# Kernel tuning notes

Measured on AMD Instinct MI355X. Metric: run time of the kernel, lower is better.

The kernel has to match this reference:

```python
import jax, jax.numpy as jnp
import numpy as np

TOP_K = 2
EPS = 1e-20


def setup_inputs() -> dict:
    key = jax.random.key(0)
    ks = jax.random.split(key, 8)
    B, S, H, E, D = 4, 2048, 1024, 8, 2048
    s = 0.02
    return {
        "x":  jax.random.normal(ks[0], (B, S, H), dtype=jnp.float32),
        "Wr": jax.random.normal(ks[1], (H, E), dtype=jnp.float32) * s,
        "Wg": jax.random.normal(ks[2], (E, H, D), dtype=jnp.float32) * s,
        "Wu": jax.random.normal(ks[3], (E, H, D), dtype=jnp.float32) * s,
        "Wd": jax.random.normal(ks[4], (E, D, H), dtype=jnp.float32) * s,
        "Sg": jax.random.normal(ks[5], (H, D), dtype=jnp.float32) * s,
        "Su": jax.random.normal(ks[6], (H, D), dtype=jnp.float32) * s,
        "Sd": jax.random.normal(ks[7], (D, H), dtype=jnp.float32) * s,
    }


def reference(x, Wr, Wg, Wu, Wd, Sg, Su, Sd):
    B, S, H = x.shape
    T = B * S
    xt = x.reshape(T, H)

    # Router: softmax scores, top-k, renormalize top-k weights
    scores = jax.nn.softmax(xt @ Wr, axis=-1)            # [T, E]
    topk_w, topk_idx = jax.lax.top_k(scores, TOP_K)      # [T, K]
    topk_w = topk_w / (topk_w.sum(axis=-1, keepdims=True) + EPS)

    # Per-expert SwiGLU FFN computed densely over all tokens (vectorized over E)
    g = jax.nn.silu(jnp.einsum('th,ehd->etd', xt, Wg))   # [E, T, D]
    u = jnp.einsum('th,ehd->etd', xt, Wu)                # [E, T, D]
    out_all = jnp.einsum('etd,edh->eth', g * u, Wd)      # [E, T, H]

    # Combine: gather each token's top-k expert outputs, weighted sum
    tok = jnp.arange(T)[:, None]                          # [T, 1]
    gathered = out_all[topk_idx, tok, :]                  # [T, K, H]
    out = jnp.sum(gathered * topk_w[..., None], axis=1).reshape(B, S, H)

    # Shared expert (applied to original input, added to MoE output)
    shared = (jax.nn.silu(x @ Sg) * (x @ Su)) @ Sd        # [B, S, H]
    return out + shared
```

## Files before the change

### kernel.cpp

```cpp
#include <hip/hip_runtime.h>
#include <stdint.h>

#define T_TOK 8192
#define HD 1024
#define ED 8
#define DD 2048
#define BM 128
#define BK 32
#define TILE_SHARED 64
#define TILE_MAX 200
#define ROWCAP 25600
#define RT_TPW 8

typedef short short8 __attribute__((ext_vector_type(8)));
typedef float f32x4 __attribute__((ext_vector_type(4)));

__device__ __forceinline__ unsigned short f2bf(float f) {
  union { float f; unsigned int u; } v; v.f = f;
  unsigned int r = (v.u + 0x7fffu + ((v.u >> 16) & 1u)) >> 16;
  return (unsigned short)r;
}

__device__ __forceinline__ void gll16(const void* g, void* l) {
  __builtin_amdgcn_global_load_lds(
      (const __attribute__((address_space(1))) unsigned int*)g,
      (__attribute__((address_space(3))) unsigned int*)l, 16, 0, 0);
}

__global__ __launch_bounds__(256) void k_zero(float* __restrict__ outp) {
  size_t i = (size_t)blockIdx.x * 256 + threadIdx.x;
  ((float4*)outp)[i] = make_float4(0.f, 0.f, 0.f, 0.f);
}

__global__ __launch_bounds__(256) void k_init(int* counts, int* tok, float* wrow) {
  int i = blockIdx.x * 256 + threadIdx.x;
  if (i < 32) counts[i] = 0;
  if (i < ROWCAP) {
    tok[i] = (i < T_TOK) ? i : 0;
    wrow[i] = (i < T_TOK) ? 1.0f : 0.0f;
  }
}

__global__ __launch_bounds__(256) void k_transpose(const float* __restrict__ in,
    unsigned short* __restrict__ outp, int R, int C) {
  __shared__ float tile[32][33];
  size_t boff = (size_t)blockIdx.z * (size_t)R * (size_t)C;
  in += boff; outp += boff;
  int c0 = blockIdx.x * 32, r0 = blockIdx.y * 32;
  int tx = threadIdx.x & 31, ty = threadIdx.x >> 5;
#pragma unroll
  for (int i = 0; i < 4; ++i)
    tile[ty + i * 8][tx] = in[(size_t)(r0 + ty + i * 8) * C + c0 + tx];
  __syncthreads();
#pragma unroll
  for (int i = 0; i < 4; ++i)
    outp[(size_t)(c0 + ty + i * 8) * R + r0 + tx] = f2bf(tile[tx][ty + i * 8]);
}

__global__ __launch_bounds__(256) void k_router(const float* __restrict__ x,
    const float* __restrict__ Wr, unsigned short* __restrict__ xb,
    int* __restrict__ counts, int* __restrict__ topE, float* __restrict__ topW) {
  __shared__ float wrT[ED * HD];
  __shared__ int hist[ED];
  int tid = threadIdx.x;
  if (tid < ED) hist[tid] = 0;
  for (int i = tid; i < ED * HD; i += 256) {
    int e = i >> 10, h = i & (HD - 1);
    wrT[i] = Wr[h * ED + e];
  }
  __syncthreads();
  int lane = tid & 63, wave = tid >> 6;
  int tbase = (blockIdx.x * 4 + wave) * RT_TPW;
  for (int tt = 0; tt < RT_TPW; ++tt) {
    int t = tbase + tt;
    const float* xrow = x + (size_t)t * HD;
    unsigned short* xbrow = xb + (size_t)t * HD;
    float acc[ED] = {0, 0, 0, 0, 0, 0, 0, 0};
#pragma unroll
    for (int i = 0; i < HD / 64; ++i) {
      int h = i * 64 + lane;
      float v = xrow[h];
      xbrow[h] = f2bf(v);
#pragma unroll
      for (int e = 0; e < ED; ++e) acc[e] += v * wrT[e * HD + h];
    }
#pragma unroll
    for (int off = 32; off; off >>= 1)
#pragma unroll
      for (int e = 0; e < ED; ++e) acc[e] += __shfl_xor(acc[e], off);
    if (lane == 0) {
      float m = acc[0];
#pragma unroll
      for (int e = 1; e < ED; ++e) m = fmaxf(m, acc[e]);
      float p[ED], s = 0.f;
#pragma unroll
      for (int e = 0; e < ED; ++e) { p[e] = __expf(acc[e] - m); s += p[e]; }
      int i0 = 0;
#pragma unroll
      for (int e = 1; e < ED; ++e) if (acc[e] > acc[i0]) i0 = e;
      int i1 = -1;
#pragma unroll
      for (int e = 0; e < ED; ++e) {
        if (e == i0) continue;
        if (i1 < 0 || acc[e] > acc[i1]) i1 = e;
      }
      float p0 = p[i0] / s, p1 = p[i1] / s;
      float rs = p0 + p1 + 1e-20f;
      topE[t * 2] = i0; topE[t * 2 + 1] = i1;
      topW[t * 2] = p0 / rs; topW[t * 2 + 1] = p1 / rs;
      atomicAdd(&hist[i0], 1);
      atomicAdd(&hist[i1], 1);
    }
  }
  __syncthreads();
  if (tid < ED) atomicAdd(&counts[tid], hist[tid]);
}

__global__ __launch_bounds__(256) void k_plan(const int* __restrict__ counts, int* cursor,
    int* __restrict__ tileE, int* __restrict__ tileEnd) {
  __shared__ int tstart[ED + 1], segend[ED];
  if (threadIdx.x == 0) {
    int base = T_TOK, rt = TILE_SHARED;
    for (int e = 0; e < ED; ++e) {
      int c = counts[e];
      cursor[e] = base;
      tstart[e] = rt;
      segend[e] = base + c;
      int tiles = (c + BM - 1) >> 7;
      rt += tiles;
      base += tiles << 7;
    }
    tstart[ED] = rt;
  }
  __syncthreads();
  for (int rt = threadIdx.x; rt < TILE_MAX; rt += 256) {
    int e = -1, end = 0;
    if (rt < TILE_SHARED) { e = ED; end = T_TOK; }
    else {
      for (int q = 0; q < ED; ++q)
        if (rt >= tstart[q] && rt < tstart[q + 1]) { e = q; end = segend[q]; }
    }
    tileE[rt] = e; tileEnd[rt] = end;
  }
}

__global__ __launch_bounds__(256) void k_scatter(const int* __restrict__ topE,
    const float* __restrict__ topW, int* cursor, int* tok, float* wrow) {
  __shared__ int lcount[ED], lbase[ED];
  int tid = threadIdx.x;
  if (tid < ED) lcount[tid] = 0;
  __syncthreads();
  int t = blockIdx.x * 256 + tid;
  int e0 = topE[t * 2], e1 = topE[t * 2 + 1];
  float w0 = topW[t * 2], w1 = topW[t * 2 + 1];
  int s0 = atomicAdd(&lcount[e0], 1);
  int s1 = atomicAdd(&lcount[e1], 1);
  __syncthreads();
  if (tid < ED) lbase[tid] = atomicAdd(&cursor[tid], lcount[tid]);
  __syncthreads();
  int p0 = lbase[e0] + s0;
  int p1 = lbase[e1] + s1;
  tok[p0] = t; wrow[p0] = w0;
  tok[p1] = t; wrow[p1] = w1;
}


__global__ __launch_bounds__(256, 2) void k_gemm1(
    const unsigned short* __restrict__ xb,
    const unsigned short* __restrict__ wgt, const unsigned short* __restrict__ wut,
    const unsigned short* __restrict__ sgt, const unsigned short* __restrict__ sut,
    const int* __restrict__ tok, const int* __restrict__ tileE,
    const int* __restrict__ tileEnd, unsigned short* __restrict__ hbuf, int tileBase) {
  int lt = blockIdx.y;
  int rt = tileBase + lt;
  int e = tileE[rt];
  if (e < 0) return;
  int n0 = blockIdx.x * BM;
  int grow0 = rt * BM;
  int hrow0 = lt * BM;
  int segEnd = tileEnd[rt];
  const unsigned short* bg = (e == ED) ? sgt : wgt + (size_t)e * DD * HD;
  const unsigned short* bu = (e == ED) ? sut : wut + (size_t)e * DD * HD;

  __shared__ __align__(16) unsigned short As[2][BM * BK];
  __shared__ __align__(16) unsigned short Bg[2][BM * BK];
  __shared__ __align__(16) unsigned short Bu[2][BM * BK];

  int tid = threadIdx.x, lane = tid & 63, wave = tid >> 6;
  int wm = (wave & 1) * 64, wn = (wave >> 1) * 64;
  int kc = (lane & 3) ^ ((lane >> 3) & 3);

  int ldsU[2];
  const unsigned short *pA[2], *pBg[2], *pBu[2];
#pragma unroll
  for (int r = 0; r < 2; ++r) {
    int chunk = r * 4 + wave;
    int row = chunk * 16 + (lane >> 2);
    ldsU[r] = chunk * 512;
    pA[r]  = xb + (size_t)tok[grow0 + row] * HD + kc * 8;
    pBg[r] = bg + (size_t)(n0 + row) * HD + kc * 8;
    pBu[r] = bu + (size_t)(n0 + row) * HD + kc * 8;
  }

  f32x4 zero = {0.f, 0.f, 0.f, 0.f};
  f32x4 accg[4][4], accu[4][4];
#pragma unroll
  for (int i = 0; i < 4; ++i)
#pragma unroll
    for (int j = 0; j < 4; ++j) { accg[i][j] = zero; accu[i][j] = zero; }

  int m15 = lane & 15;
  int sl8 = (((lane >> 4) ^ ((lane >> 1) & 3)) * 8);

#pragma unroll
  for (int r = 0; r < 2; ++r) {
    gll16(pA[r],  &As[0][ldsU[r]]);
    gll16(pBg[r], &Bg[0][ldsU[r]]);
    gll16(pBu[r], &Bu[0][ldsU[r]]);
  }
  __syncthreads();

  for (int k0 = 0; k0 < HD; k0 += BK) {
    int b = (k0 >> 5) & 1;
    int k1 = k0 + BK;
    if (k1 < HD) {
#pragma unroll
      for (int r = 0; r < 2; ++r) {
        gll16(pA[r] + k1,  &As[b ^ 1][ldsU[r]]);
        gll16(pBg[r] + k1, &Bg[b ^ 1][ldsU[r]]);
        gll16(pBu[r] + k1, &Bu[b ^ 1][ldsU[r]]);
      }
    }
    __builtin_amdgcn_sched_barrier(0);
    short8 af[4], bgf[4], buf_[4];
#pragma unroll
    for (int i = 0; i < 4; ++i) {
      af[i]   = *(const short8*)(&As[b][(wm + i * 16 + m15) * BK + sl8]);
      bgf[i]  = *(const short8*)(&Bg[b][(wn + i * 16 + m15) * BK + sl8]);
      buf_[i] = *(const short8*)(&Bu[b][(wn + i * 16 + m15) * BK + sl8]);
    }
#pragma unroll
    for (int i = 0; i < 4; ++i)
#pragma unroll
      for (int j = 0; j < 4; ++j) {
        accg[i][j] = __builtin_amdgcn_mfma_f32_16x16x32_bf16(af[i], bgf[j],  accg[i][j], 0, 0, 0);
        accu[i][j] = __builtin_amdgcn_mfma_f32_16x16x32_bf16(af[i], buf_[j], accu[i][j], 0, 0, 0);
      }
    __syncthreads();
  }

  int colB = n0 + wn + m15;
  int rowB = wm + ((lane >> 4) << 2);
#pragma unroll
  for (int i = 0; i < 4; ++i)
#pragma unroll
    for (int j = 0; j < 4; ++j)
#pragma unroll
      for (int r = 0; r < 4; ++r) {
        int lr = rowB + i * 16 + r;
        float g = accg[i][j][r], u = accu[i][j][r];
        float h = (grow0 + lr < segEnd) ? (g / (1.0f + __expf(-g))) * u : 0.0f;
        hbuf[(size_t)(hrow0 + lr) * DD + colB + j * 16] = f2bf(h);
      }
}

__global__ __launch_bounds__(256, 2) void k_gemm2(
    const unsigned short* __restrict__ hbuf,
    const unsigned short* __restrict__ wdt, const unsigned short* __restrict__ sdt,
    const int* __restrict__ tok, const int* __restrict__ tileE,
    const int* __restrict__ tileEnd, const float* __restrict__ wrow,
    float* __restrict__ outp, int tileBase) {
  int lt = blockIdx.y;
  int rt = tileBase + lt;
  int e = tileE[rt];
  if (e < 0) return;
  int n0 = blockIdx.x * BM;
  int grow0 = rt * BM;
  int hrow0 = lt * BM;
  int segEnd = tileEnd[rt];
  const unsigned short* bd = (e == ED) ? sdt : wdt + (size_t)e * HD * DD;

  __shared__ __align__(16) unsigned short As[2][BM * BK];
  __shared__ __align__(16) unsigned short Bs[2][BM * BK];

  int tid = threadIdx.x, lane = tid & 63, wave = tid >> 6;
  int wm = (wave & 1) * 64, wn = (wave >> 1) * 64;
  int kc = (lane & 3) ^ ((lane >> 3) & 3);

  int ldsU[2];
  const unsigned short *pA[2], *pB[2];
#pragma unroll
  for (int r = 0; r < 2; ++r) {
    int chunk = r * 4 + wave;
    int row = chunk * 16 + (lane >> 2);
    ldsU[r] = chunk * 512;
    pA[r] = hbuf + (size_t)(hrow0 + row) * DD + kc * 8;
    pB[r] = bd + (size_t)(n0 + row) * DD + kc * 8;
  }

  f32x4 zero = {0.f, 0.f, 0.f, 0.f};
  f32x4 acc[4][4];
#pragma unroll
  for (int i = 0; i < 4; ++i)
#pragma unroll
    for (int j = 0; j < 4; ++j) acc[i][j] = zero;

  int m15 = lane & 15;
  int sl8 = (((lane >> 4) ^ ((lane >> 1) & 3)) * 8);

#pragma unroll
  for (int r = 0; r < 2; ++r) {
    gll16(pA[r], &As[0][ldsU[r]]);
    gll16(pB[r], &Bs[0][ldsU[r]]);
  }
  __syncthreads();

  for (int k0 = 0; k0 < DD; k0 += BK) {
    int b = (k0 >> 5) & 1;
    int k1 = k0 + BK;
    if (k1 < DD) {
#pragma unroll
      for (int r = 0; r < 2; ++r) {
        gll16(pA[r] + k1, &As[b ^ 1][ldsU[r]]);
        gll16(pB[r] + k1, &Bs[b ^ 1][ldsU[r]]);
      }
    }
    __builtin_amdgcn_sched_barrier(0);
    short8 af[4], bf[4];
#pragma unroll
    for (int i = 0; i < 4; ++i) {
      af[i] = *(const short8*)(&As[b][(wm + i * 16 + m15) * BK + sl8]);
      bf[i] = *(const short8*)(&Bs[b][(wn + i * 16 + m15) * BK + sl8]);
    }
#pragma unroll
    for (int i = 0; i < 4; ++i)
#pragma unroll
      for (int j = 0; j < 4; ++j)
        acc[i][j] = __builtin_amdgcn_mfma_f32_16x16x32_bf16(af[i], bf[j], acc[i][j], 0, 0, 0);
    __syncthreads();
  }

  int colB = n0 + wn + m15;
  int rowB = wm + ((lane >> 4) << 2);
#pragma unroll
  for (int i = 0; i < 4; ++i)
#pragma unroll
    for (int r = 0; r < 4; ++r) {
      int grr = grow0 + rowB + i * 16 + r;
      if (grr < segEnd) {
        float w = wrow[grr];
        size_t ob = (size_t)tok[grr] * HD;
#pragma unroll
        for (int j = 0; j < 4; ++j)
          atomicAdd(&outp[ob + colB + j * 16], acc[i][j][r] * w);
      }
    }
}

extern "C" void kernel_launch(void* const* d_in, const int* in_sizes, int n_in,
                              void* d_out, int out_size, void* d_ws, size_t ws_size,
                              hipStream_t stream) {
  const float* x  = (const float*)d_in[0];
  const float* Wr = (const float*)d_in[1];
  const float* Wg = (const float*)d_in[2];
  const float* Wu = (const float*)d_in[3];
  const float* Wd = (const float*)d_in[4];
  const float* Sg = (const float*)d_in[5];
  const float* Su = (const float*)d_in[6];
  const float* Sd = (const float*)d_in[7];
  float* outp = (float*)d_out;

  size_t fixed = 0;
  auto pad = [](size_t b) { return (b + 255) & ~(size_t)255; };
  fixed += pad((size_t)T_TOK * HD * 2);
  fixed += pad((size_t)ED * DD * HD * 2) * 3;
  fixed += pad((size_t)DD * HD * 2) * 3;
  fixed += pad((size_t)ROWCAP * 4) * 2;
  fixed += pad((size_t)T_TOK * 2 * 4) * 2;
  fixed += pad(128) * 2 + pad(1024) * 2;
  int CH = TILE_MAX;
  if (fixed + pad((size_t)CH * BM * DD * 2) > ws_size) CH = TILE_MAX / 2;
  if (fixed + pad((size_t)CH * BM * DD * 2) > ws_size) return;

  char* ws = (char*)d_ws;
  size_t off = 0;
  auto alloc = [&](size_t bytes) -> char* {
    char* p = ws + off;
    off += (bytes + 255) & ~(size_t)255;
    return p;
  };
  unsigned short* xb  = (unsigned short*)alloc((size_t)T_TOK * HD * 2);
  unsigned short* wgt = (unsigned short*)alloc((size_t)ED * DD * HD * 2);
  unsigned short* wut = (unsigned short*)alloc((size_t)ED * DD * HD * 2);
  unsigned short* wdt = (unsigned short*)alloc((size_t)ED * HD * DD * 2);
  unsigned short* sgt = (unsigned short*)alloc((size_t)DD * HD * 2);
  unsigned short* sut = (unsigned short*)alloc((size_t)DD * HD * 2);
  unsigned short* sdt = (unsigned short*)alloc((size_t)HD * DD * 2);
  int* tok       = (int*)alloc((size_t)ROWCAP * 4);
  float* wrow    = (float*)alloc((size_t)ROWCAP * 4);
  int* topE      = (int*)alloc((size_t)T_TOK * 2 * 4);
  float* topW    = (float*)alloc((size_t)T_TOK * 2 * 4);
  int* counts    = (int*)alloc(128);
  int* cursor    = (int*)alloc(128);
  int* tileE     = (int*)alloc(1024);
  int* tileEnd   = (int*)alloc(1024);
  unsigned short* hbuf = (unsigned short*)alloc((size_t)CH * BM * DD * 2);

  k_zero<<<(out_size / 4 + 255) / 256, 256, 0, stream>>>(outp);
  k_init<<<(ROWCAP + 255) / 256, 256, 0, stream>>>(counts, tok, wrow);
  k_transpose<<<dim3(DD / 32, HD / 32, ED), 256, 0, stream>>>(Wg, wgt, HD, DD);
  k_transpose<<<dim3(DD / 32, HD / 32, ED), 256, 0, stream>>>(Wu, wut, HD, DD);
  k_transpose<<<dim3(HD / 32, DD / 32, ED), 256, 0, stream>>>(Wd, wdt, DD, HD);
  k_transpose<<<dim3(DD / 32, HD / 32, 1), 256, 0, stream>>>(Sg, sgt, HD, DD);
  k_transpose<<<dim3(DD / 32, HD / 32, 1), 256, 0, stream>>>(Su, sut, HD, DD);
  k_transpose<<<dim3(HD / 32, DD / 32, 1), 256, 0, stream>>>(Sd, sdt, DD, HD);
  k_router<<<T_TOK / (4 * RT_TPW), 256, 0, stream>>>(x, Wr, xb, counts, topE, topW);
  k_plan<<<1, 256, 0, stream>>>(counts, cursor, tileE, tileEnd);
  k_scatter<<<T_TOK / 256, 256, 0, stream>>>(topE, topW, cursor, tok, wrow);
  for (int cb = 0; cb < TILE_MAX; cb += CH) {
    k_gemm1<<<dim3(DD / BM, CH), 256, 0, stream>>>(xb, wgt, wut, sgt, sut, tok,
                                                   tileE, tileEnd, hbuf, cb);
    k_gemm2<<<dim3(HD / BM, CH), 256, 0, stream>>>(hbuf, wdt, sdt, tok, tileE,
                                                   tileEnd, wrow, outp, cb);
  }
}
```

Baseline: 768.1 us.

## Triple-buffer LDS tiles with two-stage prefetch and explicit vmcnt waits

Both GEMM kernels move from double to triple buffering of LDS tiles. Each iteration issues loads two K-steps ahead, and the per-iteration double __syncthreads is replaced by one partial s_waitcnt vmcnt followed by a single s_barrier. The aim is to keep more global-to-LDS loads in flight and to cut the synchronization stalls between loading and the MFMA work. In exchange, LDS use per block grows by half, which may limit occupancy under launch_bounds(256,2). The hand-written vmcnt counts must also match the number of loads issued.

```diff
diff --git a/kernel.cpp b/kernel.cpp
--- a/kernel.cpp
+++ b/kernel.cpp
@@ -182,9 +182,9 @@
   const unsigned short* bg = (e == ED) ? sgt : wgt + (size_t)e * DD * HD;
   const unsigned short* bu = (e == ED) ? sut : wut + (size_t)e * DD * HD;
 
-  __shared__ __align__(16) unsigned short As[2][BM * BK];
-  __shared__ __align__(16) unsigned short Bg[2][BM * BK];
-  __shared__ __align__(16) unsigned short Bu[2][BM * BK];
+  __shared__ __align__(16) unsigned short As[3][BM * BK];
+  __shared__ __align__(16) unsigned short Bg[3][BM * BK];
+  __shared__ __align__(16) unsigned short Bu[3][BM * BK];
 
   int tid = threadIdx.x, lane = tid & 63, wave = tid >> 6;
   int wm = (wave & 1) * 64, wn = (wave >> 1) * 64;
@@ -218,17 +218,29 @@
     gll16(pBg[r], &Bg[0][ldsU[r]]);
     gll16(pBu[r], &Bu[0][ldsU[r]]);
   }
-  __syncthreads();
+#pragma unroll
+  for (int r = 0; r < 2; ++r) {
+    gll16(pA[r] + BK,  &As[1][ldsU[r]]);
+    gll16(pBg[r] + BK, &Bg[1][ldsU[r]]);
+    gll16(pBu[r] + BK, &Bu[1][ldsU[r]]);
+  }
 
   for (int k0 = 0; k0 < HD; k0 += BK) {
-    int b = (k0 >> 5) & 1;
-    int k1 = k0 + BK;
-    if (k1 < HD) {
+    int ti = k0 >> 5;
+    int b  = ti % 3;
+    if (k0 + BK < HD) asm volatile("s_waitcnt vmcnt(6)" ::: "memory");
+    else              asm volatile("s_waitcnt vmcnt(0)" ::: "memory");
+    __builtin_amdgcn_sched_barrier(0);
+    __builtin_amdgcn_s_barrier();
+    __builtin_amdgcn_sched_barrier(0);
+    int k2 = k0 + 2 * BK;
+    if (k2 < HD) {
+      int b2 = (ti + 2) % 3;
 #pragma unroll
       for (int r = 0; r < 2; ++r) {
-        gll16(pA[r] + k1,  &As[b ^ 1][ldsU[r]]);
-        gll16(pBg[r] + k1, &Bg[b ^ 1][ldsU[r]]);
-        gll16(pBu[r] + k1, &Bu[b ^ 1][ldsU[r]]);
+        gll16(pA[r] + k2,  &As[b2][ldsU[r]]);
+        gll16(pBg[r] + k2, &Bg[b2][ldsU[r]]);
+        gll16(pBu[r] + k2, &Bu[b2][ldsU[r]]);
       }
     }
     __builtin_amdgcn_sched_barrier(0);
@@ -246,7 +258,7 @@
         accg[i][j] = __builtin_amdgcn_mfma_f32_16x16x32_bf16(af[i], bgf[j],  accg[i][j], 0, 0, 0);
         accu[i][j] = __builtin_amdgcn_mfma_f32_16x16x32_bf16(af[i], buf_[j], accu[i][j], 0, 0, 0);
       }
-    __syncthreads();
+    __builtin_amdgcn_sched_barrier(0);
   }
 
   int colB = n0 + wn + m15;
@@ -280,8 +292,8 @@
   int segEnd = tileEnd[rt];
   const unsigned short* bd = (e == ED) ? sdt : wdt + (size_t)e * HD * DD;
 
-  __shared__ __align__(16) unsigned short As[2][BM * BK];
-  __shared__ __align__(16) unsigned short Bs[2][BM * BK];
+  __shared__ __align__(16) unsigned short As[3][BM * BK];
+  __shared__ __align__(16) unsigned short Bs[3][BM * BK];
 
   int tid = threadIdx.x, lane = tid & 63, wave = tid >> 6;
   int wm = (wave & 1) * 64, wn = (wave >> 1) * 64;
@@ -313,16 +325,27 @@
     gll16(pA[r], &As[0][ldsU[r]]);
     gll16(pB[r], &Bs[0][ldsU[r]]);
   }
-  __syncthreads();
+#pragma unroll
+  for (int r = 0; r < 2; ++r) {
+    gll16(pA[r] + BK, &As[1][ldsU[r]]);
+    gll16(pB[r] + BK, &Bs[1][ldsU[r]]);
+  }
 
   for (int k0 = 0; k0 < DD; k0 += BK) {
-    int b = (k0 >> 5) & 1;
-    int k1 = k0 + BK;
-    if (k1 < DD) {
+    int ti = k0 >> 5;
+    int b  = ti % 3;
+    if (k0 + BK < DD) asm volatile("s_waitcnt vmcnt(4)" ::: "memory");
+    else              asm volatile("s_waitcnt vmcnt(0)" ::: "memory");
+    __builtin_amdgcn_sched_barrier(0);
+    __builtin_amdgcn_s_barrier();
+    __builtin_amdgcn_sched_barrier(0);
+    int k2 = k0 + 2 * BK;
+    if (k2 < DD) {
+      int b2 = (ti + 2) % 3;
 #pragma unroll
       for (int r = 0; r < 2; ++r) {
-        gll16(pA[r] + k1, &As[b ^ 1][ldsU[r]]);
-        gll16(pB[r] + k1, &Bs[b ^ 1][ldsU[r]]);
+        gll16(pA[r] + k2, &As[b2][ldsU[r]]);
+        gll16(pB[r] + k2, &Bs[b2][ldsU[r]]);
       }
     }
     __builtin_amdgcn_sched_barrier(0);
@@ -337,7 +360,7 @@
 #pragma unroll
       for (int j = 0; j < 4; ++j)
         acc[i][j] = __builtin_amdgcn_mfma_f32_16x16x32_bf16(af[i], bf[j], acc[i][j], 0, 0, 0);
-    __syncthreads();
+    __builtin_amdgcn_sched_barrier(0);
   }
 
   int colB = n0 + wn + m15;
```

Result: slower. 812.0 us (+5.7%).
